# Performance work log

Hardware: AMD Instinct MI355X
Metric: run time of the kernel (lower is better)

Reference implementation:

```python
import jax, jax.numpy as jnp
import numpy as np

MAX_DISP = 4  # max_displacement = pad_size = 4, stride_1 = stride_2 = 1, kernel_size = 1
NEG_SLOPE = 0.1


def setup_inputs() -> dict:
    key = jax.random.key(0)
    k1, k2 = jax.random.split(key)
    B, C, H, W = 8, 128, 128, 256
    x1 = jax.random.normal(k1, (B, C, H, W), dtype=jnp.float32)
    x2 = jax.random.normal(k2, (B, C, H, W), dtype=jnp.float32)
    return {"x1": x1, "x2": x2}


def reference(x1, x2):
    # FlowNet/PWC-Net correlation: for each displacement (dy, dx) in
    # [-MAX_DISP, MAX_DISP]^2, dot-product over channels (normalized by C),
    # giving (2*MAX_DISP+1)^2 = 81 output channels; then LeakyReLU(0.1).
    B, C, H, W = x1.shape
    pad = MAX_DISP
    x2p = jnp.pad(x2, ((0, 0), (0, 0), (pad, pad), (pad, pad)))  # [B,C,H+8,W+8]
    vols = []
    for dy in range(2 * MAX_DISP + 1):          # fixed small displacement set
        for dx in range(2 * MAX_DISP + 1):
            shifted = jax.lax.dynamic_slice(x2p, (0, 0, dy, dx), (B, C, H, W))
            vols.append(jnp.mean(x1 * shifted, axis=1))  # mean over channels
    cv = jnp.stack(vols, axis=1)                 # [B, 81, H, W]
    return jax.nn.leaky_relu(cv, NEG_SLOPE)
```

## Files before the change

### kernel.cpp

```cpp
#include <hip/hip_runtime.h>


constexpr int MAXD = 4;
constexpr int ND   = 9;
constexpr int NDISP = 81;
constexpr int Bb = 8, Cc = 128, Hh = 128, Ww = 256;
constexpr int TH = 8, TW = 64, NPIX = 8;
constexpr int NTHREADS = ND * 64;
constexpr int HW = Hh * Ww;
constexpr float SCALE = 1.0f / 128.0f;
constexpr float SLOPE = 0.1f;

__global__ __launch_bounds__(NTHREADS, 1)
void corr81_kernel(const float* __restrict__ x1, const float* __restrict__ x2,
                   float* __restrict__ out) {
  const int tid = threadIdx.x;
  const int wv  = tid >> 6;
  const int l   = tid & 63;
  const int r   = l >> 3;
  const int cb  = (l & 7) << 3;

  const int w0 = blockIdx.x * TW;
  const int h0 = blockIdx.y * TH;
  const int b  = blockIdx.z;

  const int x1base = (b * Cc * Hh + h0 + r) * Ww + w0 + cb;

  const int gh2 = h0 + r + wv - MAXD;
  const bool rowok = (gh2 >= 0) && (gh2 < Hh);
  const int gw2 = w0 + cb - MAXD;
  bool ok[4];
#pragma unroll
  for (int s = 0; s < 4; ++s) {
    const int c0 = gw2 + 4 * s;
    ok[s] = rowok && (c0 >= 0) && (c0 + 3 < Ww);
  }
  const int ghc = rowok ? gh2 : 0;
  const int x2base = b * (Cc * HW) + ghc * Ww + gw2;

  float acc[ND][NPIX];
#pragma unroll
  for (int dx = 0; dx < ND; ++dx)
#pragma unroll
    for (int i = 0; i < NPIX; ++i) acc[dx][i] = 0.0f;

  auto ldx1 = [&](int ch, float* dst) {
    const float* p = x1 + x1base + ch * HW;
    float4 t0 = *reinterpret_cast<const float4*>(p);
    float4 t1 = *reinterpret_cast<const float4*>(p + 4);
    dst[0] = t0.x; dst[1] = t0.y; dst[2] = t0.z; dst[3] = t0.w;
    dst[4] = t1.x; dst[5] = t1.y; dst[6] = t1.z; dst[7] = t1.w;
  };
  auto ldx2 = [&](int ch, float* dst) {
    const float* p = x2 + x2base + ch * HW;
#pragma unroll
    for (int s = 0; s < 4; ++s) {
      float4 q = make_float4(0.0f, 0.0f, 0.0f, 0.0f);
      if (ok[s]) q = *reinterpret_cast<const float4*>(p + 4 * s);
      dst[4 * s + 0] = q.x; dst[4 * s + 1] = q.y;
      dst[4 * s + 2] = q.z; dst[4 * s + 3] = q.w;
    }
  };

  float a0[NPIX], a1[NPIX], xa[16], xb[16];

#define FMA_BLOCK(av, xv)                                   \
  _Pragma("unroll")                                         \
  for (int dx = 0; dx < ND; ++dx)                           \
    _Pragma("unroll")                                       \
    for (int i = 0; i < NPIX; ++i)                          \
      acc[dx][i] = fmaf((av)[i], (xv)[i + dx], acc[dx][i]);

  ldx1(0, a0);
  ldx2(0, xa);

#pragma unroll 1
  for (int ch = 0; ch < Cc; ch += 2) {
    ldx1(ch + 1, a1);
    ldx2(ch + 1, xb);
    FMA_BLOCK(a0, xa)
    if (ch + 2 < Cc) {
      ldx1(ch + 2, a0);
      ldx2(ch + 2, xa);
    }
    FMA_BLOCK(a1, xb)
  }
#undef FMA_BLOCK

  const int obase = (b * NDISP + wv * ND) * HW + (h0 + r) * Ww + w0 + cb;
#pragma unroll
  for (int dx = 0; dx < ND; ++dx) {
    float4 v0, v1;
    float t;
    t = acc[dx][0] * SCALE; v0.x = fmaxf(t, t * SLOPE);
    t = acc[dx][1] * SCALE; v0.y = fmaxf(t, t * SLOPE);
    t = acc[dx][2] * SCALE; v0.z = fmaxf(t, t * SLOPE);
    t = acc[dx][3] * SCALE; v0.w = fmaxf(t, t * SLOPE);
    t = acc[dx][4] * SCALE; v1.x = fmaxf(t, t * SLOPE);
    t = acc[dx][5] * SCALE; v1.y = fmaxf(t, t * SLOPE);
    t = acc[dx][6] * SCALE; v1.z = fmaxf(t, t * SLOPE);
    t = acc[dx][7] * SCALE; v1.w = fmaxf(t, t * SLOPE);
    float* po = out + obase + dx * HW;
    *reinterpret_cast<float4*>(po)     = v0;
    *reinterpret_cast<float4*>(po + 4) = v1;
  }
}

extern "C" void kernel_launch(void* const* d_in, const int* in_sizes, int n_in,
                              void* d_out, int out_size, void* d_ws, size_t ws_size,
                              hipStream_t stream) {
  const float* x1 = (const float*)d_in[0];
  const float* x2 = (const float*)d_in[1];
  float* out = (float*)d_out;
  dim3 grid(Ww / TW, Hh / TH, Bb);
  corr81_kernel<<<grid, NTHREADS, 0, stream>>>(x1, x2, out);
}
```

Baseline: 445.0 us.

## Stage x1/x2 tiles through LDS with async global_load_lds quad-buffered pipeline

Measured after the change: 419.4 us. -5.8%, faster.

```diff
diff --git a/kernel.cpp b/kernel.cpp
--- a/kernel.cpp
+++ b/kernel.cpp
@@ -6,8 +6,18 @@
 constexpr int NDISP = 81;
 constexpr int Bb = 8, Cc = 128, Hh = 128, Ww = 256;
 constexpr int TH = 8, TW = 64, NPIX = 8;
+constexpr int CK = 2;
+constexpr int NCHUNK = Cc / CK;
+constexpr int X2ROWS = TH + 2 * MAXD;
+constexpr int X2COLS = 72;
+constexpr int X2T = X2ROWS * X2COLS;
+constexpr int X1T = TH * TW;
+constexpr int X2R = CK * X2T;
+constexpr int CHF = CK * (X2T + X1T);
+constexpr int NBUF = 4;
 constexpr int NTHREADS = ND * 64;
 constexpr int HW = Hh * Ww;
+constexpr int CHSTRIDE = CK * HW;
 constexpr float SCALE = 1.0f / 128.0f;
 constexpr float SLOPE = 0.1f;
 
@@ -24,19 +34,73 @@
   const int h0 = blockIdx.y * TH;
   const int b  = blockIdx.z;
 
-  const int x1base = (b * Cc * Hh + h0 + r) * Ww + w0 + cb;
+  __shared__ __align__(16) float lds[NBUF * CHF];
 
-  const int gh2 = h0 + r + wv - MAXD;
-  const bool rowok = (gh2 >= 0) && (gh2 < Hh);
-  const int gw2 = w0 + cb - MAXD;
-  bool ok[4];
+  const int jn = (wv < 4) ? 2 : 1;
+  const float* src[2];
+  int  grp[2], zofs[2];
+  bool val[2];
 #pragma unroll
-  for (int s = 0; s < 4; ++s) {
-    const int c0 = gw2 + 4 * s;
-    ok[s] = rowok && (c0 >= 0) && (c0 + 3 < Ww);
+  for (int j = 0; j < 2; ++j) {
+    const int g = (wv < 4) ? (2 * wv + j) : (8 + (wv - 4));
+    grp[j] = g;
+    const int f = 256 * g + 4 * l;
+    bool v = true;
+    const float* p;
+    if (f < X2R) {
+      const int ch  = f / X2T;
+      const int rem = f - ch * X2T;
+      const int row = rem / X2COLS;
+      const int col = rem - row * X2COLS;
+      const int gr = h0 - MAXD + row;
+      const int gc = w0 - MAXD + col;
+      v = (gr >= 0) && (gr < Hh) && (gc >= 0) && (gc <= Ww - 4);
+      const int grc = gr < 0 ? 0 : (gr > Hh - 1 ? Hh - 1 : gr);
+      const int gcc = gc < 0 ? 0 : (gc > Ww - 4 ? Ww - 4 : gc);
+      p = x2 + ((b * Cc + ch) * HW + grc * Ww + gcc);
+    } else {
+      const int f2  = f - X2R;
+      const int ch  = f2 / X1T;
+      const int rem = f2 - ch * X1T;
+      const int row = rem >> 6;
+      const int col = rem & 63;
+      p = x1 + ((b * Cc + ch) * HW + (h0 + row) * Ww + (w0 + col));
+    }
+    src[j] = p; val[j] = v; zofs[j] = 256 * g + 4 * l;
   }
-  const int ghc = rowok ? gh2 : 0;
-  const int x2base = b * (Cc * HW) + ghc * Ww + gw2;
+
+  auto stage = [&](int kc) {
+    const int bb = (kc & (NBUF - 1)) * CHF;
+#pragma unroll
+    for (int j = 0; j < 2; ++j)
+      if (j < jn)
+        __builtin_amdgcn_global_load_lds(
+            (const __attribute__((address_space(1))) void*)(src[j] + kc * CHSTRIDE),
+            (__attribute__((address_space(3))) void*)(&lds[bb + 256 * grp[j]]),
+            16, 0, 0);
+  };
+  auto fixz = [&](int kc) {
+    const int bb = (kc & (NBUF - 1)) * CHF;
+#pragma unroll
+    for (int j = 0; j < 2; ++j)
+      if (j < jn && !val[j])
+        *reinterpret_cast<float4*>(&lds[bb + zofs[j]]) = make_float4(0.f, 0.f, 0.f, 0.f);
+  };
+  auto wait2 = [&]() { if (wv < 4) asm volatile("s_waitcnt vmcnt(4)" ::: "memory");
+                       else        asm volatile("s_waitcnt vmcnt(2)" ::: "memory"); };
+  auto wait1 = [&]() { if (wv < 4) asm volatile("s_waitcnt vmcnt(2)" ::: "memory");
+                       else        asm volatile("s_waitcnt vmcnt(1)" ::: "memory"); };
+  auto wait0 = [&]() { asm volatile("s_waitcnt vmcnt(0)" ::: "memory"); };
+  auto bar = [&]() {
+    asm volatile("s_waitcnt lgkmcnt(0)" ::: "memory");
+    __builtin_amdgcn_s_barrier();
+    asm volatile("" ::: "memory");
+  };
+
+  stage(0); stage(1); stage(2);
+  wait2();
+  fixz(0);
+  bar();
 
   float acc[ND][NPIX];
 #pragma unroll
@@ -44,48 +108,39 @@
 #pragma unroll
     for (int i = 0; i < NPIX; ++i) acc[dx][i] = 0.0f;
 
-  auto ldx1 = [&](int ch, float* dst) {
-    const float* p = x1 + x1base + ch * HW;
-    float4 t0 = *reinterpret_cast<const float4*>(p);
-    float4 t1 = *reinterpret_cast<const float4*>(p + 4);
-    dst[0] = t0.x; dst[1] = t0.y; dst[2] = t0.z; dst[3] = t0.w;
-    dst[4] = t1.x; dst[5] = t1.y; dst[6] = t1.z; dst[7] = t1.w;
-  };
-  auto ldx2 = [&](int ch, float* dst) {
-    const float* p = x2 + x2base + ch * HW;
+#pragma unroll 1
+  for (int k = 0; k < NCHUNK; ++k) {
+    if (k + 3 < NCHUNK) stage(k + 3);
+
+    const int bb = (k & (NBUF - 1)) * CHF;
 #pragma unroll
-    for (int s = 0; s < 4; ++s) {
-      float4 q = make_float4(0.0f, 0.0f, 0.0f, 0.0f);
-      if (ok[s]) q = *reinterpret_cast<const float4*>(p + 4 * s);
-      dst[4 * s + 0] = q.x; dst[4 * s + 1] = q.y;
-      dst[4 * s + 2] = q.z; dst[4 * s + 3] = q.w;
+    for (int c = 0; c < CK; ++c) {
+      const float* xp = &lds[bb + c * X2T + (r + wv) * X2COLS + cb];
+      float4 q0 = *reinterpret_cast<const float4*>(xp);
+      float4 q1 = *reinterpret_cast<const float4*>(xp + 4);
+      float4 q2 = *reinterpret_cast<const float4*>(xp + 8);
+      float4 q3 = *reinterpret_cast<const float4*>(xp + 12);
+      const float* ap = &lds[bb + X2R + c * X1T + r * TW + cb];
+      float4 t0 = *reinterpret_cast<const float4*>(ap);
+      float4 t1 = *reinterpret_cast<const float4*>(ap + 4);
+      const float xr[16] = {q0.x, q0.y, q0.z, q0.w, q1.x, q1.y, q1.z, q1.w,
+                            q2.x, q2.y, q2.z, q2.w, q3.x, q3.y, q3.z, q3.w};
+      const float av[8]  = {t0.x, t0.y, t0.z, t0.w, t1.x, t1.y, t1.z, t1.w};
+#pragma unroll
+      for (int dx = 0; dx < ND; ++dx)
+#pragma unroll
+        for (int i = 0; i < NPIX; ++i)
+          acc[dx][i] = fmaf(av[i], xr[i + dx], acc[dx][i]);
     }
-  };
 
-  float a0[NPIX], a1[NPIX], xa[16], xb[16];
-
-#define FMA_BLOCK(av, xv)                                   \
-  _Pragma("unroll")                                         \
-  for (int dx = 0; dx < ND; ++dx)                           \
-    _Pragma("unroll")                                       \
-    for (int i = 0; i < NPIX; ++i)                          \
-      acc[dx][i] = fmaf((av)[i], (xv)[i + dx], acc[dx][i]);
-
-  ldx1(0, a0);
-  ldx2(0, xa);
-
-#pragma unroll 1
-  for (int ch = 0; ch < Cc; ch += 2) {
-    ldx1(ch + 1, a1);
-    ldx2(ch + 1, xb);
-    FMA_BLOCK(a0, xa)
-    if (ch + 2 < Cc) {
-      ldx1(ch + 2, a0);
-      ldx2(ch + 2, xa);
+    if (k + 1 < NCHUNK) {
+      if      (k + 3 < NCHUNK) wait2();
+      else if (k + 2 < NCHUNK) wait1();
+      else                     wait0();
+      fixz(k + 1);
+      bar();
     }
-    FMA_BLOCK(a1, xb)
   }
-#undef FMA_BLOCK
 
   const int obase = (b * NDISP + wv * ND) * HW + (h0 + r) * Ww + w0 + cb;
 #pragma unroll
```
